# Performance work log

Measured on AMD Instinct MI355X. Metric: run time of the kernel, lower is better.

Reference implementation:

```python
import jax, jax.numpy as jnp
import numpy as np

CHUNK = 32
PRIOR = 64
POSE = 512
PRED = 128
B = 2048


def setup_inputs() -> dict:
    key = jax.random.key(0)
    k1, k2, k3, k4, k5, k6 = jax.random.split(key, 6)
    initial_feature = jax.random.normal(k1, (B, PRIOR, POSE), dtype=jnp.float32)
    pred_feature = jax.random.normal(k2, (B, PRED, POSE), dtype=jnp.float32)
    s1 = 1.0 / np.sqrt(CHUNK * POSE)
    s2 = 1.0 / np.sqrt(POSE)
    W1 = jax.random.uniform(k3, (POSE, CHUNK * POSE), minval=-s1, maxval=s1, dtype=jnp.float32)
    b1 = jax.random.uniform(k4, (POSE,), minval=-s1, maxval=s1, dtype=jnp.float32)
    W2 = jax.random.uniform(k5, (POSE, POSE), minval=-s2, maxval=s2, dtype=jnp.float32)
    b2 = jax.random.uniform(k6, (POSE,), minval=-s2, maxval=s2, dtype=jnp.float32)
    return {"initial_feature": initial_feature, "pred_feature": pred_feature,
            "W1": W1, "b1": b1, "W2": W2, "b2": b2}


def reference(initial_feature, pred_feature, W1, b1, W2, b2):
    Bn = initial_feature.shape[0]
    # last CHUNK prior frames flattened -> [B, CHUNK*POSE]
    x = initial_feature[:, PRIOR - CHUNK:, :].reshape(Bn, -1)
    # spatial_chunk_encoder (Dropout is identity in eval mode)
    mem = (x @ W1.T + b1) @ W2.T + b2          # [B, POSE]
    head = pred_feature[:, :CHUNK, :]          # [B, CHUNK, POSE]
    score = jnp.einsum('bd,bcd->bc', mem, head)  # per-token dot product
    g = jax.nn.sigmoid(score)[..., None]       # [B, CHUNK, 1]
    blended = g * head + (1.0 - g) * mem[:, None, :]
    return pred_feature.at[:, :CHUNK, :].set(blended)
```

## Files before the change

kernel.cpp:

```cpp
#include <hip/hip_runtime.h>
#include <hip/hip_bf16.h>
#include <stdint.h>

#define CHUNKC 32
#define PRIORC 64
#define POSEC 512
#define PREDC 128
#define NB 2048
#define K1 (CHUNKC*POSEC)
#define KS 16
#define KCH (K1/KS)

typedef __attribute__((ext_vector_type(8))) short bf16x8;
typedef __attribute__((ext_vector_type(8))) unsigned short u16x8;
typedef __attribute__((ext_vector_type(4))) float f32x4;
typedef __attribute__((ext_vector_type(4))) float f4v;
typedef __attribute__((ext_vector_type(4))) unsigned short u16x4;

__device__ __forceinline__ unsigned short f2b(float f) {
    union { float f; unsigned int u; } x; x.f = f;
    unsigned int r = x.u + 0x7fffu + ((x.u >> 16) & 1u);
    return (unsigned short)(r >> 16);
}
__device__ __forceinline__ float b2f(unsigned short u) {
    union { unsigned int i; float f; } x; x.i = ((unsigned int)u) << 16; return x.f;
}

__device__ __forceinline__ void gload_lds16(const void* g, void* l) {
    __builtin_amdgcn_global_load_lds(
        (const __attribute__((address_space(1))) unsigned int*)g,
        (__attribute__((address_space(3))) unsigned int*)l, 16, 0, 0);
}

#define XN4   8388608
#define W1N4  2097152
#define W2N4  65536
__global__ __launch_bounds__(256) void cvt_all_kernel(const float4* __restrict__ init,
                                                      const float4* __restrict__ W1,
                                                      const float4* __restrict__ W2,
                                                      ushort4* __restrict__ xb,
                                                      ushort4* __restrict__ w1b,
                                                      ushort4* __restrict__ w2b) {
    const int64_t n = XN4 + W1N4 + W2N4;
    const int64_t stride = (int64_t)gridDim.x * blockDim.x;
    for (int64_t i = (int64_t)blockIdx.x * blockDim.x + threadIdx.x; i < n; i += stride) {
        float4 v; ushort4* dst;
        if (i < XN4) {
            int64_t b = i >> 12, r = i & 4095;
            v = init[b * 8192 + 4096 + r];
            dst = xb + i;
        } else if (i < XN4 + W1N4) {
            v = W1[i - XN4];
            dst = w1b + (i - XN4);
        } else {
            v = W2[i - XN4 - W1N4];
            dst = w2b + (i - XN4 - W1N4);
        }
        *dst = make_ushort4(f2b(v.x), f2b(v.y), f2b(v.z), f2b(v.w));
    }
}

__global__ __launch_bounds__(512) void gemm1_kernel(const ushort* __restrict__ xb,
                                                    const ushort* __restrict__ w1b,
                                                    ushort* __restrict__ part) {
    __shared__ ushort As[2][256][64];
    __shared__ ushort Bs[2][256][64];
    const int t = threadIdx.x;
    const int l = t & 63, wid = t >> 6;
    const int wr = wid >> 2, wc = wid & 3;
    const int cpx = 256 >> 3;
    const int orig = (blockIdx.x & 7) * cpx + (blockIdx.x >> 3);
    const int mt = orig & 7, nt = (orig >> 3) & 1, ks = orig >> 4;
    const int NIT = KCH / 64;

    f32x4 acc[8][4] = {};

    const ushort* aG = xb  + (int64_t)(mt * 256) * K1 + ks * KCH;
    const ushort* bG = w1b + (int64_t)(nt * 256) * K1 + ks * KCH;
    const int srow = t >> 3;
    const int scol = (((t & 7) ^ ((t >> 3) & 7))) * 8;

    const int fr = l & 15, fq = l >> 4;
    const int cx = fr & 7;

#pragma unroll
    for (int i = 0; i < 4; ++i) {
        gload_lds16(aG + (int64_t)(i * 64 + srow) * K1 + scol,
                    (char*)&As[0][0][0] + i * 8192 + wid * 1024);
        gload_lds16(bG + (int64_t)(i * 64 + srow) * K1 + scol,
                    (char*)&Bs[0][0][0] + i * 8192 + wid * 1024);
    }

    for (int it = 0; it < NIT; ++it) {
        const int cur = it & 1;
        __syncthreads();
        if (it + 1 < NIT) {
            const int nxt = cur ^ 1;
            const int k0 = (it + 1) * 64;
#pragma unroll
            for (int i = 0; i < 4; ++i) {
                gload_lds16(aG + (int64_t)(i * 64 + srow) * K1 + k0 + scol,
                            (char*)&As[nxt][0][0] + i * 8192 + wid * 1024);
                gload_lds16(bG + (int64_t)(i * 64 + srow) * K1 + k0 + scol,
                            (char*)&Bs[nxt][0][0] + i * 8192 + wid * 1024);
            }
        }
#pragma unroll
        for (int k2 = 0; k2 < 2; ++k2) {
            const int cs = ((k2 * 4 + fq) ^ cx) * 8;
            bf16x8 a[8], b[4];
#pragma unroll
            for (int m = 0; m < 8; ++m)
                a[m] = *(const bf16x8*)&As[cur][wr * 128 + m * 16 + fr][cs];
#pragma unroll
            for (int n = 0; n < 4; ++n)
                b[n] = *(const bf16x8*)&Bs[cur][wc * 64 + n * 16 + fr][cs];
#pragma unroll
            for (int m = 0; m < 8; ++m)
#pragma unroll
                for (int n = 0; n < 4; ++n)
                    acc[m][n] = __builtin_amdgcn_mfma_f32_16x16x32_bf16(a[m], b[n], acc[m][n], 0, 0, 0);
        }
    }

    ushort* P = part + (int64_t)ks * NB * POSEC;
    const int mbase = mt * 256 + wr * 128, nbase = nt * 256 + wc * 64;
#pragma unroll
    for (int m = 0; m < 8; ++m)
#pragma unroll
        for (int n = 0; n < 4; ++n) {
            int row0 = mbase + m * 16 + fq * 4;
            int col  = nbase + n * 16 + fr;
#pragma unroll
            for (int r = 0; r < 4; ++r)
                P[(int64_t)(row0 + r) * POSEC + col] = f2b(acc[m][n][r]);
        }
}

__global__ __launch_bounds__(256) void reduce_kernel(const ushort* __restrict__ part,
                                                     const float* __restrict__ b1,
                                                     u16x8* __restrict__ A2) {
    const int gid = blockIdx.x * 256 + threadIdx.x;
    const int64_t e0 = (int64_t)gid * 8;
    float s[8] = {};
#pragma unroll
    for (int k = 0; k < KS; ++k) {
        u16x8 p = *(const u16x8*)(part + (int64_t)k * (NB * POSEC) + e0);
#pragma unroll
        for (int j = 0; j < 8; ++j) s[j] += b2f(p[j]);
    }
    const int col = (int)(e0 & 511);
    f4v b0 = *(const f4v*)&b1[col];
    f4v b4 = *(const f4v*)&b1[col + 4];
    u16x8 o;
#pragma unroll
    for (int j = 0; j < 4; ++j) { o[j] = f2b(s[j] + b0[j]); o[j+4] = f2b(s[j+4] + b4[j]); }
    A2[gid] = o;
}

__global__ __launch_bounds__(256) void gemm2_kernel(const ushort* __restrict__ A2,
                                                    const ushort* __restrict__ w2b,
                                                    const float* __restrict__ b2,
                                                    float* __restrict__ mem) {
    __shared__ ushort As[64][64];
    __shared__ ushort Bs[64][64];
    const int t = threadIdx.x;
    const int l = t & 63, wid = t >> 6;
    const int wr = wid >> 1, wc = wid & 1;
    const int mt = blockIdx.x >> 3, nt = blockIdx.x & 7;

    f32x4 acc[2][2] = {};
    const ushort* aG = A2  + (int64_t)(mt * 64) * POSEC;
    const ushort* bG = w2b + (int64_t)(nt * 64) * POSEC;
    const int srow = t >> 3;
    const int scol = (((t & 7) ^ ((t >> 3) & 7))) * 8;
    const int fr = l & 15, fq = l >> 4;
    const int cx = fr & 7;

    for (int k0 = 0; k0 < POSEC; k0 += 64) {
#pragma unroll
        for (int i = 0; i < 2; ++i) {
            gload_lds16(aG + (int64_t)(i * 32 + srow) * POSEC + k0 + scol,
                        (char*)&As[0][0] + i * 4096 + wid * 1024);
            gload_lds16(bG + (int64_t)(i * 32 + srow) * POSEC + k0 + scol,
                        (char*)&Bs[0][0] + i * 4096 + wid * 1024);
        }
        __syncthreads();
#pragma unroll
        for (int k2 = 0; k2 < 2; ++k2) {
            const int cs = ((k2 * 4 + fq) ^ cx) * 8;
            bf16x8 a[2], b[2];
#pragma unroll
            for (int m = 0; m < 2; ++m)
                a[m] = *(const bf16x8*)&As[wr * 32 + m * 16 + fr][cs];
#pragma unroll
            for (int n = 0; n < 2; ++n)
                b[n] = *(const bf16x8*)&Bs[wc * 32 + n * 16 + fr][cs];
#pragma unroll
            for (int m = 0; m < 2; ++m)
#pragma unroll
                for (int n = 0; n < 2; ++n)
                    acc[m][n] = __builtin_amdgcn_mfma_f32_16x16x32_bf16(a[m], b[n], acc[m][n], 0, 0, 0);
        }
        __syncthreads();
    }

    const int mbase = mt * 64 + wr * 32, nbase = nt * 64 + wc * 32;
#pragma unroll
    for (int m = 0; m < 2; ++m)
#pragma unroll
        for (int n = 0; n < 2; ++n) {
            int row0 = mbase + m * 16 + fq * 4;
            int col  = nbase + n * 16 + fr;
            float bias = b2[col];
#pragma unroll
            for (int r = 0; r < 4; ++r)
                mem[(int64_t)(row0 + r) * POSEC + col] = acc[m][n][r] + bias;
        }
}

__global__ __launch_bounds__(256) void blend_kernel(const float* __restrict__ pred,
                                                    const float* __restrict__ mem,
                                                    float* __restrict__ out) {
    const int b = blockIdx.x;
    const int t = threadIdx.x;
    __shared__ float sm[POSEC];
    __shared__ float sg[CHUNKC];

    sm[t]       = mem[(int64_t)b * POSEC + t];
    sm[t + 256] = mem[(int64_t)b * POSEC + 256 + t];
    __syncthreads();

    const int l = t & 63, wid = t >> 6;
    const float4* sm4 = (const float4*)sm;
    const float4* p4 = (const float4*)pred + (int64_t)b * 16384;
    float4* o4 = (float4*)out + (int64_t)b * 16384;

#pragma unroll
    for (int ci = 0; ci < 8; ++ci) {
        int c = wid * 8 + ci;
        float4 h0 = p4[c * 128 + l * 2];
        float4 h1 = p4[c * 128 + l * 2 + 1];
        float4 m0 = sm4[l * 2];
        float4 m1 = sm4[l * 2 + 1];
        float s = h0.x * m0.x + h0.y * m0.y + h0.z * m0.z + h0.w * m0.w
                + h1.x * m1.x + h1.y * m1.y + h1.z * m1.z + h1.w * m1.w;
#pragma unroll
        for (int o = 32; o; o >>= 1) s += __shfl_xor(s, o);
        if (l == 0) sg[c] = 1.0f / (1.0f + expf(-s));
    }
    __syncthreads();

#pragma unroll
    for (int i = 0; i < 16; ++i) {
        int idx = i * 256 + t;
        int row = idx >> 7, c4 = idx & 127;
        float g = sg[row];
        float4 h = p4[idx];
        float4 m = sm4[c4];
        float4 r;
        r.x = g * h.x + (1.0f - g) * m.x;
        r.y = g * h.y + (1.0f - g) * m.y;
        r.z = g * h.z + (1.0f - g) * m.z;
        r.w = g * h.w + (1.0f - g) * m.w;
        o4[idx] = r;
    }
#pragma unroll
    for (int i = 0; i < 48; ++i) {
        int idx = 4096 + i * 256 + t;
        f4v h = __builtin_nontemporal_load((const f4v*)p4 + idx);
        __builtin_nontemporal_store(h, (f4v*)o4 + idx);
    }
}


extern "C" void kernel_launch(void* const* d_in, const int* in_sizes, int n_in,
                              void* d_out, int out_size, void* d_ws, size_t ws_size,
                              hipStream_t stream) {
    const float* init = (const float*)d_in[0];
    const float* pred = (const float*)d_in[1];
    const float* W1   = (const float*)d_in[2];
    const float* b1   = (const float*)d_in[3];
    const float* W2   = (const float*)d_in[4];
    const float* b2   = (const float*)d_in[5];
    float* out = (float*)d_out;

    char* ws = (char*)d_ws;
    ushort* xb   = (ushort*)(ws);
    ushort* w1b  = (ushort*)(ws + 67108864);
    ushort* w2b  = (ushort*)(ws + 83886080);
    ushort* part = (ushort*)(ws + 84410368);
    ushort* A2   = (ushort*)(ws + 117964800);
    float*  mem  = (float*) (ws + 120061952);

    cvt_all_kernel<<<2560, 256, 0, stream>>>((const float4*)init, (const float4*)W1,
                                             (const float4*)W2,
                                             (ushort4*)xb, (ushort4*)w1b, (ushort4*)w2b);
    gemm1_kernel<<<256, 512, 0, stream>>>(xb, w1b, part);
    reduce_kernel<<<512, 256, 0, stream>>>(part, b1, (u16x8*)A2);
    gemm2_kernel<<<256, 256, 0, stream>>>(A2, w2b, b2, mem);
    blend_kernel<<<NB, 256, 0, stream>>>(pred, mem, out);
}
```

Measured before the change: 319.7 us.

## Fuse activation fp32-to-bf16 conversion into gemm1 and halve split-K

Removes the separate pass that converted the 128 MB slice of initial_feature to bf16. gemm1 now streams fp32 activations straight into LDS with a swizzled layout and converts them to bf16 in registers before the MFMA. The M tile drops from 256 to 128 rows and split-K goes from 16 to 8, which keeps the same 256 blocks while halving the partial-sum traffic. The trade-off is more LDS bytes per A element, conversion ALU work inside the inner loop, and lower MFMA reuse per block.

```diff
diff --git a/kernel.cpp b/kernel.cpp
--- a/kernel.cpp
+++ b/kernel.cpp
@@ -8,14 +8,13 @@
 #define PREDC 128
 #define NB 2048
 #define K1 (CHUNKC*POSEC)
-#define KS 16
+#define KS 8
 #define KCH (K1/KS)
 
 typedef __attribute__((ext_vector_type(8))) short bf16x8;
 typedef __attribute__((ext_vector_type(8))) unsigned short u16x8;
 typedef __attribute__((ext_vector_type(4))) float f32x4;
 typedef __attribute__((ext_vector_type(4))) float f4v;
-typedef __attribute__((ext_vector_type(4))) unsigned short u16x4;
 
 __device__ __forceinline__ unsigned short f2b(float f) {
     union { float f; unsigned int u; } x; x.f = f;
@@ -25,6 +24,10 @@
 __device__ __forceinline__ float b2f(unsigned short u) {
     union { unsigned int i; float f; } x; x.i = ((unsigned int)u) << 16; return x.f;
 }
+__device__ __forceinline__ unsigned short cf(float f) {
+    __hip_bfloat16 h = __float2bfloat16(f);
+    union { __hip_bfloat16 h; unsigned short u; } x; x.h = h; return x.u;
+}
 
 __device__ __forceinline__ void gload_lds16(const void* g, void* l) {
     __builtin_amdgcn_global_load_lds(
@@ -32,62 +35,52 @@
         (__attribute__((address_space(3))) unsigned int*)l, 16, 0, 0);
 }
 
-#define XN4   8388608
 #define W1N4  2097152
 #define W2N4  65536
-__global__ __launch_bounds__(256) void cvt_all_kernel(const float4* __restrict__ init,
-                                                      const float4* __restrict__ W1,
-                                                      const float4* __restrict__ W2,
-                                                      ushort4* __restrict__ xb,
-                                                      ushort4* __restrict__ w1b,
-                                                      ushort4* __restrict__ w2b) {
-    const int64_t n = XN4 + W1N4 + W2N4;
+__global__ __launch_bounds__(256) void cvt_w_kernel(const float4* __restrict__ W1,
+                                                    const float4* __restrict__ W2,
+                                                    ushort4* __restrict__ w1b,
+                                                    ushort4* __restrict__ w2b) {
+    const int64_t n = W1N4 + W2N4;
     const int64_t stride = (int64_t)gridDim.x * blockDim.x;
     for (int64_t i = (int64_t)blockIdx.x * blockDim.x + threadIdx.x; i < n; i += stride) {
         float4 v; ushort4* dst;
-        if (i < XN4) {
-            int64_t b = i >> 12, r = i & 4095;
-            v = init[b * 8192 + 4096 + r];
-            dst = xb + i;
-        } else if (i < XN4 + W1N4) {
-            v = W1[i - XN4];
-            dst = w1b + (i - XN4);
-        } else {
-            v = W2[i - XN4 - W1N4];
-            dst = w2b + (i - XN4 - W1N4);
-        }
+        if (i < W1N4) { v = W1[i]; dst = w1b + i; }
+        else          { v = W2[i - W1N4]; dst = w2b + (i - W1N4); }
         *dst = make_ushort4(f2b(v.x), f2b(v.y), f2b(v.z), f2b(v.w));
     }
 }
 
-__global__ __launch_bounds__(512) void gemm1_kernel(const ushort* __restrict__ xb,
+__global__ __launch_bounds__(512) void gemm1_kernel(const float* __restrict__ init,
                                                     const ushort* __restrict__ w1b,
                                                     ushort* __restrict__ part) {
-    __shared__ ushort As[2][256][64];
+    __shared__ float  As[2][128][64];
     __shared__ ushort Bs[2][256][64];
     const int t = threadIdx.x;
     const int l = t & 63, wid = t >> 6;
     const int wr = wid >> 2, wc = wid & 3;
-    const int cpx = 256 >> 3;
-    const int orig = (blockIdx.x & 7) * cpx + (blockIdx.x >> 3);
-    const int mt = orig & 7, nt = (orig >> 3) & 1, ks = orig >> 4;
+    const int orig = (blockIdx.x & 7) * 32 + (blockIdx.x >> 3);
+    const int mt = orig & 15, nt = (orig >> 4) & 1, ks = orig >> 5;
     const int NIT = KCH / 64;
 
-    f32x4 acc[8][4] = {};
-
-    const ushort* aG = xb  + (int64_t)(mt * 256) * K1 + ks * KCH;
+    f32x4 acc[4][4] = {};
+
+    const float*  aG = init + (int64_t)(mt * 128) * 32768 + 16384 + ks * KCH;
     const ushort* bG = w1b + (int64_t)(nt * 256) * K1 + ks * KCH;
-    const int srow = t >> 3;
-    const int scol = (((t & 7) ^ ((t >> 3) & 7))) * 8;
+
+    const int arow  = t >> 4;
+    const int aslot = (t & 15) ^ ((t >> 4) & 15);
+    const int brow = t >> 3;
+    const int bcol = ((t & 7) ^ ((t >> 3) & 7)) * 8;
 
     const int fr = l & 15, fq = l >> 4;
-    const int cx = fr & 7;
+    const int cxB = fr & 7;
 
 #pragma unroll
     for (int i = 0; i < 4; ++i) {
-        gload_lds16(aG + (int64_t)(i * 64 + srow) * K1 + scol,
+        gload_lds16(aG + (int64_t)(i * 32 + arow) * 32768 + aslot * 4,
                     (char*)&As[0][0][0] + i * 8192 + wid * 1024);
-        gload_lds16(bG + (int64_t)(i * 64 + srow) * K1 + scol,
+        gload_lds16(bG + (int64_t)(i * 64 + brow) * K1 + bcol,
                     (char*)&Bs[0][0][0] + i * 8192 + wid * 1024);
     }
 
@@ -99,24 +92,33 @@
             const int k0 = (it + 1) * 64;
 #pragma unroll
             for (int i = 0; i < 4; ++i) {
-                gload_lds16(aG + (int64_t)(i * 64 + srow) * K1 + k0 + scol,
+                gload_lds16(aG + (int64_t)(i * 32 + arow) * 32768 + k0 + aslot * 4,
                             (char*)&As[nxt][0][0] + i * 8192 + wid * 1024);
-                gload_lds16(bG + (int64_t)(i * 64 + srow) * K1 + k0 + scol,
+                gload_lds16(bG + (int64_t)(i * 64 + brow) * K1 + k0 + bcol,
                             (char*)&Bs[nxt][0][0] + i * 8192 + wid * 1024);
             }
         }
 #pragma unroll
         for (int k2 = 0; k2 < 2; ++k2) {
-            const int cs = ((k2 * 4 + fq) ^ cx) * 8;
-            bf16x8 a[8], b[4];
-#pragma unroll
-            for (int m = 0; m < 8; ++m)
-                a[m] = *(const bf16x8*)&As[cur][wr * 128 + m * 16 + fr][cs];
+            bf16x8 a[4], b[4];
+            const int s0 = k2 * 8 + fq * 2;
+#pragma unroll
+            for (int m = 0; m < 4; ++m) {
+                const int r = wr * 64 + m * 16 + fr;
+                f32x4 va = *(const f32x4*)&As[cur][r][((s0    ) ^ fr) * 4];
+                f32x4 vb = *(const f32x4*)&As[cur][r][((s0 + 1) ^ fr) * 4];
+                u16x8 w;
+                w[0] = cf(va[0]); w[1] = cf(va[1]); w[2] = cf(va[2]); w[3] = cf(va[3]);
+                w[4] = cf(vb[0]); w[5] = cf(vb[1]); w[6] = cf(vb[2]); w[7] = cf(vb[3]);
+                union { u16x8 u; bf16x8 b; } cvtu; cvtu.u = w;
+                a[m] = cvtu.b;
+            }
+            const int cs = ((k2 * 4 + fq) ^ cxB) * 8;
 #pragma unroll
             for (int n = 0; n < 4; ++n)
                 b[n] = *(const bf16x8*)&Bs[cur][wc * 64 + n * 16 + fr][cs];
 #pragma unroll
-            for (int m = 0; m < 8; ++m)
+            for (int m = 0; m < 4; ++m)
 #pragma unroll
                 for (int n = 0; n < 4; ++n)
                     acc[m][n] = __builtin_amdgcn_mfma_f32_16x16x32_bf16(a[m], b[n], acc[m][n], 0, 0, 0);
@@ -124,9 +126,9 @@
     }
 
     ushort* P = part + (int64_t)ks * NB * POSEC;
-    const int mbase = mt * 256 + wr * 128, nbase = nt * 256 + wc * 64;
-#pragma unroll
-    for (int m = 0; m < 8; ++m)
+    const int mbase = mt * 128 + wr * 64, nbase = nt * 256 + wc * 64;
+#pragma unroll
+    for (int m = 0; m < 4; ++m)
 #pragma unroll
         for (int n = 0; n < 4; ++n) {
             int row0 = mbase + m * 16 + fq * 4;
@@ -286,17 +288,15 @@
     float* out = (float*)d_out;
 
     char* ws = (char*)d_ws;
-    ushort* xb   = (ushort*)(ws);
-    ushort* w1b  = (ushort*)(ws + 67108864);
-    ushort* w2b  = (ushort*)(ws + 83886080);
-    ushort* part = (ushort*)(ws + 84410368);
-    ushort* A2   = (ushort*)(ws + 117964800);
-    float*  mem  = (float*) (ws + 120061952);
-
-    cvt_all_kernel<<<2560, 256, 0, stream>>>((const float4*)init, (const float4*)W1,
-                                             (const float4*)W2,
-                                             (ushort4*)xb, (ushort4*)w1b, (ushort4*)w2b);
-    gemm1_kernel<<<256, 512, 0, stream>>>(xb, w1b, part);
+    ushort* w1b  = (ushort*)(ws);
+    ushort* w2b  = (ushort*)(ws + 16777216);
+    ushort* part = (ushort*)(ws + 17301504);
+    ushort* A2   = (ushort*)(ws + 34078720);
+    float*  mem  = (float*) (ws + 36175872);
+
+    cvt_w_kernel<<<1024, 256, 0, stream>>>((const float4*)W1, (const float4*)W2,
+                                           (ushort4*)w1b, (ushort4*)w2b);
+    gemm1_kernel<<<256, 512, 0, stream>>>(init, w1b, part);
     reduce_kernel<<<512, 256, 0, stream>>>(part, b1, (u16x8*)A2);
     gemm2_kernel<<<256, 256, 0, stream>>>(A2, w2b, b2, mem);
     blend_kernel<<<NB, 256, 0, stream>>>(pred, mem, out);
```

After: 295.5 us. -7.6%, faster.
